# Optimization experiments

Measured on AMD Instinct MI355X. Metric: run time of the kernel, lower is better.

## Reference

```python
import jax, jax.numpy as jnp
import numpy as np

N, E, F_IN, F_HID, F_OUT = 50000, 800000, 128, 128, 64


def setup_inputs() -> dict:
    key = jax.random.key(0)
    k_x, k_e, k_w1, k_w2 = jax.random.split(key, 4)
    x = jax.random.normal(k_x, (N, F_IN), dtype=jnp.float32)
    edge_index = jax.random.randint(k_e, (2, E), 0, N, dtype=jnp.int32)
    # GCNConv params (glorot-ish scale)
    W1 = jax.random.normal(k_w1, (F_IN, F_HID), dtype=jnp.float32) * (1.0 / np.sqrt(F_IN))
    b1 = jnp.zeros((F_HID,), dtype=jnp.float32)
    W2 = jax.random.normal(k_w2, (F_HID, F_OUT), dtype=jnp.float32) * (1.0 / np.sqrt(F_HID))
    b2 = jnp.zeros((F_OUT,), dtype=jnp.float32)
    return {"x": x, "edge_index": edge_index, "W1": W1, "b1": b1, "W2": W2, "b2": b2}


def reference(x, edge_index, W1, b1, W2, b2):
    n = x.shape[0]
    # PyG GCNConv: add self-loops, symmetric normalization deg^-1/2 * deg^-1/2
    loops = jnp.arange(n, dtype=edge_index.dtype)
    src = jnp.concatenate([edge_index[0], loops])  # (E+N,)
    dst = jnp.concatenate([edge_index[1], loops])  # (E+N,)
    deg = jax.ops.segment_sum(jnp.ones_like(dst, dtype=x.dtype), dst, num_segments=n)
    dinv = jnp.where(deg > 0, jax.lax.rsqrt(jnp.maximum(deg, 1.0)), 0.0)
    norm = dinv[src] * dinv[dst]  # (E+N,)

    def conv(h, W, b):
        h = h @ W                               # (n, f_out)
        msg = h[src] * norm[:, None]            # gather + scale, (E+N, f_out)
        return jax.ops.segment_sum(msg, dst, num_segments=n) + b

    h = jax.nn.relu(conv(x, W1, b1))  # dropout p=0.0 -> identity
    return conv(h, W2, b2)
```

## Files before the change

### kernel.cpp

```cpp
#include <hip/hip_runtime.h>

typedef __bf16 bf16x8 __attribute__((ext_vector_type(8)));
typedef float  f32x4  __attribute__((ext_vector_type(4)));

__device__ __forceinline__ float bf2f(unsigned short h) {
    return __uint_as_float(((unsigned int)h) << 16);
}
__device__ __forceinline__ unsigned short f2bf(float f) {
    unsigned int u = __float_as_uint(f);
    u += 0x7FFFu + ((u >> 16) & 1u);
    return (unsigned short)(u >> 16);
}
__device__ __forceinline__ void unpack8(uint4 u, float* v) {
    v[0] = __uint_as_float(u.x << 16); v[1] = __uint_as_float(u.x & 0xFFFF0000u);
    v[2] = __uint_as_float(u.y << 16); v[3] = __uint_as_float(u.y & 0xFFFF0000u);
    v[4] = __uint_as_float(u.z << 16); v[5] = __uint_as_float(u.z & 0xFFFF0000u);
    v[6] = __uint_as_float(u.w << 16); v[7] = __uint_as_float(u.w & 0xFFFF0000u);
}

__global__ void k1_deg_detect(const int* __restrict__ dst, int* __restrict__ deg,
                              int* __restrict__ rank, int E,
                              const unsigned short* __restrict__ x, int* __restrict__ cnt,
                              int degBlocks) {
    if ((int)blockIdx.x < degBlocks) {
        int base = blockIdx.x * 1024 + threadIdx.x;
#pragma unroll
        for (int k = 0; k < 4; ++k) {
            int e = base + k * 256;
            if (e < E) rank[e] = atomicAdd(&deg[dst[e]], 1);
        }
    } else {
        int c = 0;
        for (int i = threadIdx.x; i < 4096; i += 256) {
            unsigned e = (x[i] >> 7) & 0xFFu;
            if (e >= 0x88u) ++c;
        }
        if (c) atomicAdd(cnt, c);
    }
}

template <int COLS>
__device__ __forceinline__ void prepack_one(const void* W, unsigned short* Wp, int idx,
                                            bool isf32) {
    if (idx >= (COLS / 16) * 4 * 64) return;
    int lane = idx & 63;
    int ks   = (idx >> 6) & 3;
    int nt   = idx >> 8;
    int col  = nt * 16 + (lane & 15);
    int krow = ks * 32 + (lane >> 4) * 8;
    unsigned short tmp[8];
#pragma unroll
    for (int j = 0; j < 8; ++j) {
        size_t e = (size_t)(krow + j) * COLS + col;
        float v = isf32 ? ((const float*)W)[e] : bf2f(((const unsigned short*)W)[e]);
        tmp[j] = f2bf(v);
    }
    *(uint4*)(Wp + (size_t)idx * 8) = *(uint4*)tmp;
}

__global__ void k2_scan1_prep(const int* __restrict__ deg, int* __restrict__ offs,
                              int* __restrict__ bsum, float* __restrict__ dinv, int N, int NB,
                              const void* __restrict__ W1, const void* __restrict__ W2,
                              const void* __restrict__ b1, const void* __restrict__ b2,
                              unsigned short* __restrict__ Wp1, unsigned short* __restrict__ Wp2,
                              float* __restrict__ b1f, float* __restrict__ b2f,
                              const int* __restrict__ cnt) {
    __shared__ int s[256];
    int t = threadIdx.x;
    if ((int)blockIdx.x < NB) {
        int base = blockIdx.x * 1024 + t * 4;
        int d4[4];
#pragma unroll
        for (int k = 0; k < 4; ++k) d4[k] = (base + k < N) ? deg[base + k] : 0;
#pragma unroll
        for (int k = 0; k < 4; ++k)
            if (base + k < N) dinv[base + k] = rsqrtf((float)d4[k] + 1.0f);
        int mySum = d4[0] + d4[1] + d4[2] + d4[3];
        s[t] = mySum;
        __syncthreads();
        for (int d = 1; d < 256; d <<= 1) {
            int v = (t >= d) ? s[t - d] : 0;
            __syncthreads();
            s[t] += v;
            __syncthreads();
        }
        int run = s[t] - mySum;
#pragma unroll
        for (int k = 0; k < 4; ++k) {
            if (base + k < N) offs[base + k] = run;
            run += d4[k];
        }
        if (t == 255) bsum[blockIdx.x] = s[255];
    } else {
        bool isf32 = (*cnt >= 16);
        int bid = blockIdx.x - NB;
        if (bid < 8) {
            prepack_one<128>(W1, Wp1, bid * 256 + t, isf32);
        } else if (bid < 12) {
            prepack_one<64>(W2, Wp2, (bid - 8) * 256 + t, isf32);
        } else {
            if (t < 128) b1f[t] = isf32 ? ((const float*)b1)[t]
                                        : bf2f(((const unsigned short*)b1)[t]);
            else if (t < 192) b2f[t - 128] = isf32 ? ((const float*)b2)[t - 128]
                                                   : bf2f(((const unsigned short*)b2)[t - 128]);
        }
    }
}

__global__ void scan23(const int* __restrict__ bsum, int* __restrict__ offs,
                       int N, int E, int NB) {
    __shared__ int s[256];
    int t = threadIdx.x;
    s[t] = (t < NB) ? bsum[t] : 0;
    __syncthreads();
    for (int d = 1; d < 256; d <<= 1) {
        int v = (t >= d) ? s[t - d] : 0;
        __syncthreads();
        s[t] += v;
        __syncthreads();
    }
    int boff = (blockIdx.x > 0) ? s[blockIdx.x - 1] : 0;
    int base = blockIdx.x * 1024 + t * 4;
#pragma unroll
    for (int k = 0; k < 4; ++k) {
        int i = base + k;
        if (i < N) offs[i] += boff;
    }
    if (blockIdx.x == 0 && t == 0) offs[N] = E;
}

template <int COLS, int XMODE>
__device__ __forceinline__ void gemm_body(const void* __restrict__ X,
                                          const unsigned short* __restrict__ Wp,
                                          unsigned short* __restrict__ O, int nstrips,
                                          bool xf32f, int blockI) {
    constexpr int NT = COLS / 16;
    const int wave = threadIdx.x >> 6;
    const int lane = threadIdx.x & 63;
    const int strip = blockI * 4 + wave;
    if (strip >= nstrips) return;
    const bool xf32 = (XMODE == 0) && xf32f;
    const int m = lane & 15;
    const int q = lane >> 4;
    const size_t rowoff = (size_t)(strip * 16 + m) * 128 + q * 8;

    f32x4 acc[NT];
#pragma unroll
    for (int nt = 0; nt < NT; ++nt) acc[nt] = (f32x4){0.f, 0.f, 0.f, 0.f};

#pragma unroll
    for (int ks = 0; ks < 4; ++ks) {
        bf16x8 a;
        if (xf32) {
            const float* xp = (const float*)X + rowoff + ks * 32;
            float4 u = ((const float4*)xp)[0];
            float4 v = ((const float4*)xp)[1];
            unsigned short tmp[8];
            tmp[0] = f2bf(u.x); tmp[1] = f2bf(u.y); tmp[2] = f2bf(u.z); tmp[3] = f2bf(u.w);
            tmp[4] = f2bf(v.x); tmp[5] = f2bf(v.y); tmp[6] = f2bf(v.z); tmp[7] = f2bf(v.w);
            a = *(bf16x8*)tmp;
        } else {
            a = *(const bf16x8*)((const unsigned short*)X + rowoff + ks * 32);
        }
#pragma unroll
        for (int nt = 0; nt < NT; ++nt) {
            bf16x8 b = *(const bf16x8*)(Wp + (size_t)((nt * 4 + ks) * 64 + lane) * 8);
            acc[nt] = __builtin_amdgcn_mfma_f32_16x16x32_bf16(a, b, acc[nt], 0, 0, 0);
        }
    }

    const int r0 = strip * 16 + q * 4;
#pragma unroll
    for (int nt = 0; nt < NT; ++nt) {
#pragma unroll
        for (int r = 0; r < 4; ++r)
            O[(size_t)(r0 + r) * COLS + nt * 16 + m] = f2bf(acc[nt][r]);
    }
}

__global__ __launch_bounds__(256) void k5_gemm1_scatter(
        const void* __restrict__ X, const unsigned short* __restrict__ Wp,
        unsigned short* __restrict__ O, int nstrips, const int* __restrict__ cnt,
        int gemmBlocks,
        const int* __restrict__ src, const int* __restrict__ dst,
        const int* __restrict__ offs, const int* __restrict__ rank,
        int* __restrict__ adj, int E) {
    if ((int)blockIdx.x < gemmBlocks) {
        gemm_body<128, 0>(X, Wp, O, nstrips, (*cnt >= 16), blockIdx.x);
    } else {
        int base = (blockIdx.x - gemmBlocks) * 1024 + threadIdx.x;
#pragma unroll
        for (int k = 0; k < 4; ++k) {
            int e = base + k * 256;
            if (e < E) adj[offs[dst[e]] + rank[e]] = src[e];
        }
    }
}

__global__ __launch_bounds__(256) void gemm2_k(const void* __restrict__ X,
                                               const unsigned short* __restrict__ Wp,
                                               unsigned short* __restrict__ O, int nstrips) {
    gemm_body<64, 1>(X, Wp, O, nstrips, false, blockIdx.x);
}

__global__ void gather1(const unsigned short* __restrict__ Hb, const float* __restrict__ dinv,
                        const float* __restrict__ b, const int* __restrict__ offs,
                        const int* __restrict__ adj, unsigned short* __restrict__ R1,
                        int N) {
    int nd = blockIdx.x * 16 + (threadIdx.x >> 4);
    int lane = threadIdx.x & 63;
    int l15 = lane & 15;
    int gbase = lane & ~15;
    int f8 = l15 * 8;
    if (nd >= N) return;
    float dd = dinv[nd];
    float s2 = dd * dd;
    float hv[8], acc[8], bb[8];
    unpack8(*(const uint4*)(Hb + (size_t)nd * 128 + f8), hv);
    *(float4*)&bb[0] = *(const float4*)(b + f8);
    *(float4*)&bb[4] = *(const float4*)(b + f8 + 4);
#pragma unroll
    for (int k = 0; k < 8; ++k) acc[k] = fmaf(hv[k], s2, bb[k]);

    int beg = offs[nd], end = offs[nd + 1];
    for (int c = beg; c < end; c += 16) {
        int rem = end - c;
        int myadj = (l15 < rem) ? adj[c + l15] : nd;
#pragma unroll
        for (int t = 0; t < 16; t += 8) {
            if (t >= rem) break;
            int sI[8];
#pragma unroll
            for (int k = 0; k < 8; ++k) sI[k] = __shfl(myadj, gbase + t + k, 64);
            uint4 u[8];
#pragma unroll
            for (int k = 0; k < 8; ++k) u[k] = *(const uint4*)(Hb + (size_t)sI[k] * 128 + f8);
            float n[8];
#pragma unroll
            for (int k = 0; k < 8; ++k) n[k] = (t + k < rem) ? dinv[sI[k]] * dd : 0.f;
#pragma unroll
            for (int k = 0; k < 8; ++k) {
                float v[8];
                unpack8(u[k], v);
#pragma unroll
                for (int j = 0; j < 8; ++j) acc[j] = fmaf(v[j], n[k], acc[j]);
            }
        }
    }
    unsigned short o[8];
#pragma unroll
    for (int k = 0; k < 8; ++k) o[k] = f2bf(fmaxf(acc[k], 0.f));
    *(uint4*)(R1 + (size_t)nd * 128 + f8) = *(uint4*)o;
}

__global__ void gather2(const unsigned short* __restrict__ H2b, const float* __restrict__ dinv,
                        const float* __restrict__ b, const int* __restrict__ offs,
                        const int* __restrict__ adj, void* __restrict__ out,
                        int N, const int* __restrict__ cnt) {
    bool isf32 = (*cnt >= 16);
    int nd = blockIdx.x * 32 + (threadIdx.x >> 3);
    int lane = threadIdx.x & 63;
    int l7 = lane & 7;
    int gbase = lane & ~7;
    int f8 = l7 * 8;
    if (nd >= N) return;
    float dd = dinv[nd];
    float s2 = dd * dd;
    float hv[8], acc[8], bb[8];
    unpack8(*(const uint4*)(H2b + (size_t)nd * 64 + f8), hv);
    *(float4*)&bb[0] = *(const float4*)(b + f8);
    *(float4*)&bb[4] = *(const float4*)(b + f8 + 4);
#pragma unroll
    for (int k = 0; k < 8; ++k) acc[k] = fmaf(hv[k], s2, bb[k]);

    int beg = offs[nd], end = offs[nd + 1];
    for (int c = beg; c < end; c += 8) {
        int rem = end - c;
        int myadj = (l7 < rem) ? adj[c + l7] : nd;
        int sI[8];
#pragma unroll
        for (int k = 0; k < 8; ++k) sI[k] = __shfl(myadj, gbase + k, 64);
        uint4 u[8];
#pragma unroll
        for (int k = 0; k < 8; ++k) u[k] = *(const uint4*)(H2b + (size_t)sI[k] * 64 + f8);
        float n[8];
#pragma unroll
        for (int k = 0; k < 8; ++k) n[k] = (k < rem) ? dinv[sI[k]] * dd : 0.f;
#pragma unroll
        for (int k = 0; k < 8; ++k) {
            float v[8];
            unpack8(u[k], v);
#pragma unroll
            for (int j = 0; j < 8; ++j) acc[j] = fmaf(v[j], n[k], acc[j]);
        }
    }
    if (isf32) {
        float* op = (float*)out + (size_t)nd * 64 + f8;
        *(float4*)op       = *(float4*)&acc[0];
        *(float4*)(op + 4) = *(float4*)&acc[4];
    } else {
        unsigned short o[8];
#pragma unroll
        for (int k = 0; k < 8; ++k) o[k] = f2bf(acc[k]);
        *(uint4*)((unsigned short*)out + (size_t)nd * 64 + f8) = *(uint4*)o;
    }
}

extern "C" void kernel_launch(void* const* d_in, const int* in_sizes, int n_in,
                              void* d_out, int out_size, void* d_ws, size_t ws_size,
                              hipStream_t stream) {
    const void* x  = d_in[0];
    const int*  ei = (const int*)d_in[1];
    const void* W1 = d_in[2];
    const void* b1 = d_in[3];
    const void* W2 = d_in[4];
    const void* b2 = d_in[5];

    const int N = in_sizes[0] / 128;
    const int E = in_sizes[1] / 2;
    const int* src = ei;
    const int* dst = ei + E;

    float* ws = (float*)d_ws;
    size_t off = 0;
    auto alloc = [&](size_t n) { size_t p = off; off += (n + 15) & ~(size_t)15; return p; };
    int*   cnt    = (int*)(ws + alloc(64));
    int*   deg    = (int*)(ws + alloc(N));
    float* dinv   = ws + alloc(N);
    int*   offs   = (int*)(ws + alloc(N + 1));
    int*   bsum   = (int*)(ws + alloc(256));
    int*   adj    = (int*)(ws + alloc(E));
    int*   rank   = (int*)(ws + alloc(E));
    unsigned short* R1  = (unsigned short*)(ws + alloc((size_t)N * 64));
    unsigned short* Hb  = (unsigned short*)(ws + alloc((size_t)N * 64));
    unsigned short* Wp1 = (unsigned short*)(ws + alloc(8192));
    unsigned short* Wp2 = (unsigned short*)(ws + alloc(4096));
    float* b1f    = ws + alloc(128);
    float* b2f    = ws + alloc(64);
    unsigned short* H2b = Hb;

    hipMemsetAsync(ws, 0, (64 + ((size_t)(N + 15) & ~(size_t)15)) * sizeof(float), stream);

    const int EB = (E + 1023) / 1024;
    const int NB = (N + 1023) / 1024;
    const int nstrips = (N + 15) / 16;
    const int GB = (nstrips + 3) / 4;

    k1_deg_detect<<<EB + 1, 256, 0, stream>>>(dst, deg, rank, E,
                                              (const unsigned short*)x, cnt, EB);
    k2_scan1_prep<<<NB + 13, 256, 0, stream>>>(deg, offs, bsum, dinv, N, NB,
                                               W1, W2, b1, b2, Wp1, Wp2, b1f, b2f, cnt);
    scan23<<<NB, 256, 0, stream>>>(bsum, offs, N, E, NB);
    k5_gemm1_scatter<<<GB + EB, 256, 0, stream>>>(x, Wp1, Hb, nstrips, cnt, GB,
                                                  src, dst, offs, rank, adj, E);
    gather1<<<(N + 15) / 16, 256, 0, stream>>>(Hb, dinv, b1f, offs, adj, R1, N);
    gemm2_k<<<GB, 256, 0, stream>>>(R1, Wp2, H2b, nstrips);
    gather2<<<(N + 31) / 32, 256, 0, stream>>>(H2b, dinv, b2f, offs, adj, d_out, N, cnt);
}
```

Baseline: 221.9 us.

## Fold source dinv into GEMM epilogue and use one wave per node in gathers

The GEMM epilogues now scale each output row by its dinv, so the gathers no longer load dinv per neighbour. They simply sum pre-scaled rows and apply the destination dinv and bias once at the end. Both gather kernels switch from a sub-wave per node to a full wave per node, splitting the edge list across lane groups and combining partial sums with xor shuffles. This cuts per-edge dinv lookups and spreads long adjacency lists across more lanes. The cost is cross-lane reductions and idle lanes for low-degree nodes (average degree about 17), plus fewer nodes per block. The scatter and GEMM block order in the fused kernel is also swapped.

Result: slower. 235.3 us (+6.0%).

```diff
diff --git a/kernel.cpp b/kernel.cpp
--- a/kernel.cpp
+++ b/kernel.cpp
@@ -132,6 +132,7 @@
 template <int COLS, int XMODE>
 __device__ __forceinline__ void gemm_body(const void* __restrict__ X,
                                           const unsigned short* __restrict__ Wp,
+                                          const float* __restrict__ dinv,
                                           unsigned short* __restrict__ O, int nstrips,
                                           bool xf32f, int blockI) {
     constexpr int NT = COLS / 16;
@@ -170,65 +171,65 @@
     }
 
     const int r0 = strip * 16 + q * 4;
+    float4 dv = *(const float4*)(dinv + r0);
+    float dr[4] = {dv.x, dv.y, dv.z, dv.w};
 #pragma unroll
     for (int nt = 0; nt < NT; ++nt) {
 #pragma unroll
         for (int r = 0; r < 4; ++r)
-            O[(size_t)(r0 + r) * COLS + nt * 16 + m] = f2bf(acc[nt][r]);
-    }
-}
-
-__global__ __launch_bounds__(256) void k5_gemm1_scatter(
-        const void* __restrict__ X, const unsigned short* __restrict__ Wp,
-        unsigned short* __restrict__ O, int nstrips, const int* __restrict__ cnt,
-        int gemmBlocks,
+            O[(size_t)(r0 + r) * COLS + nt * 16 + m] = f2bf(acc[nt][r] * dr[r]);
+    }
+}
+
+__global__ __launch_bounds__(256) void k5_scatter_gemm1(
         const int* __restrict__ src, const int* __restrict__ dst,
         const int* __restrict__ offs, const int* __restrict__ rank,
-        int* __restrict__ adj, int E) {
-    if ((int)blockIdx.x < gemmBlocks) {
-        gemm_body<128, 0>(X, Wp, O, nstrips, (*cnt >= 16), blockIdx.x);
-    } else {
-        int base = (blockIdx.x - gemmBlocks) * 1024 + threadIdx.x;
+        int* __restrict__ adj, int E, int EB,
+        const void* __restrict__ X, const unsigned short* __restrict__ Wp,
+        const float* __restrict__ dinv,
+        unsigned short* __restrict__ O, int nstrips, const int* __restrict__ cnt) {
+    if ((int)blockIdx.x < EB) {
+        int base = blockIdx.x * 1024 + threadIdx.x;
 #pragma unroll
         for (int k = 0; k < 4; ++k) {
             int e = base + k * 256;
             if (e < E) adj[offs[dst[e]] + rank[e]] = src[e];
         }
+    } else {
+        gemm_body<128, 0>(X, Wp, dinv, O, nstrips, (*cnt >= 16), blockIdx.x - EB);
     }
 }
 
 __global__ __launch_bounds__(256) void gemm2_k(const void* __restrict__ X,
                                                const unsigned short* __restrict__ Wp,
+                                               const float* __restrict__ dinv,
                                                unsigned short* __restrict__ O, int nstrips) {
-    gemm_body<64, 1>(X, Wp, O, nstrips, false, blockIdx.x);
+    gemm_body<64, 1>(X, Wp, dinv, O, nstrips, false, blockIdx.x);
 }
 
 __global__ void gather1(const unsigned short* __restrict__ Hb, const float* __restrict__ dinv,
                         const float* __restrict__ b, const int* __restrict__ offs,
                         const int* __restrict__ adj, unsigned short* __restrict__ R1,
                         int N) {
-    int nd = blockIdx.x * 16 + (threadIdx.x >> 4);
+    int nd = blockIdx.x * 4 + (threadIdx.x >> 6);
+    if (nd >= N) return;
     int lane = threadIdx.x & 63;
+    int g = lane >> 4;
     int l15 = lane & 15;
     int gbase = lane & ~15;
     int f8 = l15 * 8;
-    if (nd >= N) return;
-    float dd = dinv[nd];
-    float s2 = dd * dd;
-    float hv[8], acc[8], bb[8];
-    unpack8(*(const uint4*)(Hb + (size_t)nd * 128 + f8), hv);
-    *(float4*)&bb[0] = *(const float4*)(b + f8);
-    *(float4*)&bb[4] = *(const float4*)(b + f8 + 4);
-#pragma unroll
-    for (int k = 0; k < 8; ++k) acc[k] = fmaf(hv[k], s2, bb[k]);
+
+    float acc[8];
+#pragma unroll
+    for (int k = 0; k < 8; ++k) acc[k] = 0.f;
 
     int beg = offs[nd], end = offs[nd + 1];
-    for (int c = beg; c < end; c += 16) {
-        int rem = end - c;
-        int myadj = (l15 < rem) ? adj[c + l15] : nd;
+    for (int c = beg + g * 16; c < end; c += 64) {
+        int cnt16 = end - c; if (cnt16 > 16) cnt16 = 16;
+        int myadj = (l15 < cnt16) ? adj[c + l15] : 0;
 #pragma unroll
         for (int t = 0; t < 16; t += 8) {
-            if (t >= rem) break;
+            if (t >= cnt16) break;
             int sI[8];
 #pragma unroll
             for (int k = 0; k < 8; ++k) sI[k] = __shfl(myadj, gbase + t + k, 64);
@@ -237,7 +238,7 @@
             for (int k = 0; k < 8; ++k) u[k] = *(const uint4*)(Hb + (size_t)sI[k] * 128 + f8);
             float n[8];
 #pragma unroll
-            for (int k = 0; k < 8; ++k) n[k] = (t + k < rem) ? dinv[sI[k]] * dd : 0.f;
+            for (int k = 0; k < 8; ++k) n[k] = (t + k < cnt16) ? 1.f : 0.f;
 #pragma unroll
             for (int k = 0; k < 8; ++k) {
                 float v[8];
@@ -247,36 +248,48 @@
             }
         }
     }
-    unsigned short o[8];
-#pragma unroll
-    for (int k = 0; k < 8; ++k) o[k] = f2bf(fmaxf(acc[k], 0.f));
-    *(uint4*)(R1 + (size_t)nd * 128 + f8) = *(uint4*)o;
+#pragma unroll
+    for (int k = 0; k < 8; ++k) {
+        acc[k] += __shfl_xor(acc[k], 16, 64);
+        acc[k] += __shfl_xor(acc[k], 32, 64);
+    }
+    if (g == 0) {
+        float dd = dinv[nd];
+        float hv[8], bb[8];
+        unpack8(*(const uint4*)(Hb + (size_t)nd * 128 + f8), hv);
+        *(float4*)&bb[0] = *(const float4*)(b + f8);
+        *(float4*)&bb[4] = *(const float4*)(b + f8 + 4);
+        unsigned short o[8];
+#pragma unroll
+        for (int k = 0; k < 8; ++k) {
+            float a = fmaf(acc[k] + hv[k], dd, bb[k]);
+            o[k] = f2bf(fmaxf(a, 0.f));
+        }
+        *(uint4*)(R1 + (size_t)nd * 128 + f8) = *(uint4*)o;
+    }
 }
 
 __global__ void gather2(const unsigned short* __restrict__ H2b, const float* __restrict__ dinv,
                         const float* __restrict__ b, const int* __restrict__ offs,
                         const int* __restrict__ adj, void* __restrict__ out,
                         int N, const int* __restrict__ cnt) {
+    int nd = blockIdx.x * 4 + (threadIdx.x >> 6);
+    if (nd >= N) return;
     bool isf32 = (*cnt >= 16);
-    int nd = blockIdx.x * 32 + (threadIdx.x >> 3);
     int lane = threadIdx.x & 63;
+    int g = lane >> 3;
     int l7 = lane & 7;
     int gbase = lane & ~7;
     int f8 = l7 * 8;
-    if (nd >= N) return;
-    float dd = dinv[nd];
-    float s2 = dd * dd;
-    float hv[8], acc[8], bb[8];
-    unpack8(*(const uint4*)(H2b + (size_t)nd * 64 + f8), hv);
-    *(float4*)&bb[0] = *(const float4*)(b + f8);
-    *(float4*)&bb[4] = *(const float4*)(b + f8 + 4);
-#pragma unroll
-    for (int k = 0; k < 8; ++k) acc[k] = fmaf(hv[k], s2, bb[k]);
+
+    float acc[8];
+#pragma unroll
+    for (int k = 0; k < 8; ++k) acc[k] = 0.f;
 
     int beg = offs[nd], end = offs[nd + 1];
-    for (int c = beg; c < end; c += 8) {
-        int rem = end - c;
-        int myadj = (l7 < rem) ? adj[c + l7] : nd;
+    for (int c = beg + g * 8; c < end; c += 64) {
+        int cnt8 = end - c; if (cnt8 > 8) cnt8 = 8;
+        int myadj = (l7 < cnt8) ? adj[c + l7] : 0;
         int sI[8];
 #pragma unroll
         for (int k = 0; k < 8; ++k) sI[k] = __shfl(myadj, gbase + k, 64);
@@ -285,7 +298,7 @@
         for (int k = 0; k < 8; ++k) u[k] = *(const uint4*)(H2b + (size_t)sI[k] * 64 + f8);
         float n[8];
 #pragma unroll
-        for (int k = 0; k < 8; ++k) n[k] = (k < rem) ? dinv[sI[k]] * dd : 0.f;
+        for (int k = 0; k < 8; ++k) n[k] = (k < cnt8) ? 1.f : 0.f;
 #pragma unroll
         for (int k = 0; k < 8; ++k) {
             float v[8];
@@ -294,15 +307,31 @@
             for (int j = 0; j < 8; ++j) acc[j] = fmaf(v[j], n[k], acc[j]);
         }
     }
-    if (isf32) {
-        float* op = (float*)out + (size_t)nd * 64 + f8;
-        *(float4*)op       = *(float4*)&acc[0];
-        *(float4*)(op + 4) = *(float4*)&acc[4];
-    } else {
-        unsigned short o[8];
-#pragma unroll
-        for (int k = 0; k < 8; ++k) o[k] = f2bf(acc[k]);
-        *(uint4*)((unsigned short*)out + (size_t)nd * 64 + f8) = *(uint4*)o;
+#pragma unroll
+    for (int k = 0; k < 8; ++k) {
+        acc[k] += __shfl_xor(acc[k], 8, 64);
+        acc[k] += __shfl_xor(acc[k], 16, 64);
+        acc[k] += __shfl_xor(acc[k], 32, 64);
+    }
+    if (g == 0) {
+        float dd = dinv[nd];
+        float hv[8], bb[8];
+        unpack8(*(const uint4*)(H2b + (size_t)nd * 64 + f8), hv);
+        *(float4*)&bb[0] = *(const float4*)(b + f8);
+        *(float4*)&bb[4] = *(const float4*)(b + f8 + 4);
+        float r[8];
+#pragma unroll
+        for (int k = 0; k < 8; ++k) r[k] = fmaf(acc[k] + hv[k], dd, bb[k]);
+        if (isf32) {
+            float* op = (float*)out + (size_t)nd * 64 + f8;
+            *(float4*)op       = *(float4*)&r[0];
+            *(float4*)(op + 4) = *(float4*)&r[4];
+        } else {
+            unsigned short o[8];
+#pragma unroll
+            for (int k = 0; k < 8; ++k) o[k] = f2bf(r[k]);
+            *(uint4*)((unsigned short*)out + (size_t)nd * 64 + f8) = *(uint4*)o;
+        }
     }
 }
 
@@ -351,9 +380,9 @@
     k2_scan1_prep<<<NB + 13, 256, 0, stream>>>(deg, offs, bsum, dinv, N, NB,
                                                W1, W2, b1, b2, Wp1, Wp2, b1f, b2f, cnt);
     scan23<<<NB, 256, 0, stream>>>(bsum, offs, N, E, NB);
-    k5_gemm1_scatter<<<GB + EB, 256, 0, stream>>>(x, Wp1, Hb, nstrips, cnt, GB,
-                                                  src, dst, offs, rank, adj, E);
-    gather1<<<(N + 15) / 16, 256, 0, stream>>>(Hb, dinv, b1f, offs, adj, R1, N);
-    gemm2_k<<<GB, 256, 0, stream>>>(R1, Wp2, H2b, nstrips);
-    gather2<<<(N + 31) / 32, 256, 0, stream>>>(H2b, dinv, b2f, offs, adj, d_out, N, cnt);
-}
+    k5_scatter_gemm1<<<EB + GB, 256, 0, stream>>>(src, dst, offs, rank, adj, E, EB,
+                                                  x, Wp1, dinv, Hb, nstrips, cnt);
+    gather1<<<(N + 3) / 4, 256, 0, stream>>>(Hb, dinv, b1f, offs, adj, R1, N);
+    gemm2_k<<<GB, 256, 0, stream>>>(R1, Wp2, dinv, H2b, nstrips);
+    gather2<<<(N + 3) / 4, 256, 0, stream>>>(H2b, dinv, b2f, offs, adj, d_out, N, cnt);
+}
```
